# Performance work log

Hardware: AMD Instinct MI355X
Metric: run time of the kernel (lower is better)

Reference implementation:

```python
import jax, jax.numpy as jnp
import numpy as np

B, T, I, H, O = 128, 1024, 128, 1024, 128

def setup_inputs() -> dict:
    key = jax.random.key(0)
    ks = jax.random.split(key, 11)
    s = 1.0 / np.sqrt(H)  # torch default LSTM init scale
    return {
        "x": jax.random.normal(ks[0], (B, T, I), jnp.float32),
        "sequence_length": jax.random.randint(ks[1], (B,), 0, T, jnp.int64 if jax.config.jax_enable_x64 else jnp.int32),
        "hn": jax.random.normal(ks[2], (B, H), jnp.float32),
        "cn": jax.random.normal(ks[3], (B, H), jnp.float32),
        "output_t": jax.random.normal(ks[4], (B, O), jnp.float32),
        "W_ih": jax.random.normal(ks[5], (4 * H, I + O), jnp.float32) * s,
        "W_hh": jax.random.normal(ks[6], (4 * H, H), jnp.float32) * s,
        "b_ih": jax.random.normal(ks[7], (4 * H,), jnp.float32) * s,
        "b_hh": jax.random.normal(ks[8], (4 * H,), jnp.float32) * s,
        "W_out": jax.random.normal(ks[9], (O, H), jnp.float32) * s,
        "b_out": jax.random.normal(ks[10], (O,), jnp.float32) * s,
    }

def reference(x, sequence_length, hn, cn, output_t, W_ih, W_hh, b_ih, b_hh, W_out, b_out):
    # eval mode (self.training=False): no dropout applied
    Tn = x.shape[1]
    Hd = hn.shape[-1]
    # masks[t, b] = 1.0 if sequence_length[b] > t
    masks = (jnp.arange(Tn)[:, None] < sequence_length[None, :]).astype(x.dtype)  # [T, B]
    xs = jnp.transpose(x, (1, 0, 2))  # [T, B, I]
    bias = b_ih + b_hh

    def step(carry, inp):
        h, c, out_t = carry
        xt, m = inp                      # xt [B,I], m [B]
        m = m[:, None]                   # [B,1]
        lstm_in = jnp.concatenate([xt * m, out_t], axis=-1)  # [B, I+O]
        gates = lstm_in @ W_ih.T + h @ W_hh.T + bias          # [B, 4H]
        i_g, f_g, g_g, o_g = jnp.split(gates, 4, axis=-1)     # torch gate order i,f,g,o
        i_g = jax.nn.sigmoid(i_g)
        f_g = jax.nn.sigmoid(f_g)
        g_g = jnp.tanh(g_g)
        o_g = jax.nn.sigmoid(o_g)
        c = f_g * c + i_g * g_g
        h = o_g * jnp.tanh(c)
        out_t = h @ W_out.T + b_out      # [B, O]
        return (h, c, out_t), out_t * m

    (_, _, _), ys = jax.lax.scan(step, (hn, cn, output_t), (xs, masks))
    return jnp.transpose(ys, (1, 0, 2))  # [B, T, O]
```

## Files before the change

kernel.cpp:

```cpp
#include <hip/hip_runtime.h>
#include <stdint.h>

#define Tn 1024
#define In 128

typedef __attribute__((ext_vector_type(8))) short short8;
typedef __attribute__((ext_vector_type(4))) float f32x4;
typedef unsigned long long u64;

#define WS_WFRAG  0ull
#define WS_WOUT   (WS_WFRAG + 10485760ull)
#define WS_Z0     (WS_WOUT + 262144ull)
#define WS_HBUF   (WS_Z0 + 32768ull)
#define WS_BIAS   (WS_HBUF + 524288ull)
#define WS_CNT    (WS_BIAS + 16384ull)

__device__ __forceinline__ unsigned short f2bf(float f) {
  unsigned u = __builtin_bit_cast(unsigned, f);
  return (unsigned short)((u + 0x7FFFu + ((u >> 16) & 1u)) >> 16);
}
__device__ __forceinline__ float fast_sig(float v) {
  float e = __builtin_amdgcn_exp2f(-1.44269504089f * v);
  return __builtin_amdgcn_rcpf(1.0f + e);
}
__device__ __forceinline__ float fast_tanh(float v) {
  float a = fabsf(v);
  float e = __builtin_amdgcn_exp2f(-2.88539008178f * a);
  float r = (1.0f - e) * __builtin_amdgcn_rcpf(1.0f + e);
  return copysignf(r, v);
}

__global__ void k_wfrag(const float* __restrict__ Wih, const float* __restrict__ Whh,
                        const float* __restrict__ Wout, char* __restrict__ ws) {
  const int u = blockIdx.x, nt = blockIdx.y, kt = blockIdx.z;
  const int lane = threadIdx.x;
  const int col = lane & 15, quad = lane >> 4;
  const int n = (col & 3) * 1024 + u * 32 + nt * 4 + (col >> 2);
  float v[8];
  if (kt < 32) {
    const int k = kt * 32 + quad * 8;
    #pragma unroll
    for (int e = 0; e < 8; e++) v[e] = Whh[(size_t)n * 1024 + k + e];
    const float* wo = Wih + (size_t)n * 256 + 128;
    for (int o = 0; o < 128; o++) {
      const float wv = wo[o];
      const float* wr = Wout + (size_t)o * 1024 + k;
      #pragma unroll
      for (int e = 0; e < 8; e++) v[e] = fmaf(wv, wr[e], v[e]);
    }
  } else if (kt < 36) {
    const int k = (kt - 32) * 32 + quad * 8;
    #pragma unroll
    for (int e = 0; e < 8; e++) v[e] = Wih[(size_t)n * 256 + k + e];
  } else {
    const int o = (kt - 36) * 32 + quad * 8;
    #pragma unroll
    for (int e = 0; e < 8; e++) v[e] = Wih[(size_t)n * 256 + 128 + o + e];
  }
  short8 pk;
  #pragma unroll
  for (int e = 0; e < 8; e++) pk[e] = (short)f2bf(v[e]);
  *(short8*)(ws + WS_WFRAG + ((size_t)((u * 8 + nt) * 40 + kt) * 64 + lane) * 16) = pk;
}

__global__ void k_misc(const float* __restrict__ Wout, const float* __restrict__ hn,
                       const float* __restrict__ out_t, const float* __restrict__ bout,
                       const float* __restrict__ bih, const float* __restrict__ bhh,
                       const float* __restrict__ Wih, float* __restrict__ outp,
                       char* __restrict__ ws) {
  const int blk = blockIdx.x, lane = threadIdx.x;
  const int col = lane & 15, quad = lane >> 4;
  if (blk < 256) {
    const int u = blk >> 5, kt = blk & 31;
    const int o = u * 16 + col, j0 = kt * 32 + quad * 8;
    short8 pk;
    #pragma unroll
    for (int e = 0; e < 8; e++) pk[e] = (short)f2bf(Wout[(size_t)o * 1024 + j0 + e]);
    *(short8*)(ws + WS_WOUT + ((size_t)(u * 32 + kt) * 64 + lane) * 16) = pk;
  } else if (blk < 512) {
    const int t2 = blk - 256;
    const int mm = t2 >> 5, kt = t2 & 31;
    const int b = mm * 16 + col, j0 = kt * 32 + quad * 8;
    short8 pk;
    #pragma unroll
    for (int e = 0; e < 8; e++) pk[e] = (short)f2bf(hn[(size_t)b * 1024 + j0 + e]);
    *(short8*)(ws + WS_HBUF + ((size_t)((8 + mm) * 32 + kt) * 64 + lane) * 16) = pk;
  } else if (blk < 544) {
    const int t2 = blk - 512;
    const int mm = t2 >> 2, kz = t2 & 3;
    const int b = mm * 16 + col;
    const int o0 = kz * 32 + quad * 8;
    float acc[8];
    #pragma unroll
    for (int e = 0; e < 8; e++) acc[e] = out_t[(size_t)b * 128 + o0 + e] - bout[o0 + e];
    for (int j = 0; j < 1024; j += 4) {
      const f32x4 h4 = *(const f32x4*)(hn + (size_t)b * 1024 + j);
      #pragma unroll
      for (int e = 0; e < 8; e++) {
        const f32x4 w4 = *(const f32x4*)(Wout + (size_t)(o0 + e) * 1024 + j);
        acc[e] -= h4[0] * w4[0] + h4[1] * w4[1] + h4[2] * w4[2] + h4[3] * w4[3];
      }
    }
    short8 pk;
    #pragma unroll
    for (int e = 0; e < 8; e++) pk[e] = (short)f2bf(acc[e]);
    *(short8*)(ws + WS_Z0 + ((size_t)(mm * 4 + kz) * 64 + lane) * 16) = pk;
  } else if (blk < 608) {
    const int n = (blk - 544) * 64 + lane;
    float v = bih[n] + bhh[n];
    const float* wo = Wih + (size_t)n * 256 + 128;
    for (int o = 0; o < 128; o++) v = fmaf(wo[o], bout[o], v);
    ((float*)(ws + WS_BIAS))[n] = v;
  } else if (blk < 616) {
    int* c = (int*)(ws + WS_CNT);
    const int base = ((blk - 608) * 64 + lane) * 16;
    #pragma unroll
    for (int k = 0; k < 16; k++) c[base + k] = 0;
  } else {
    int* c = (int*)outp;
    #pragma unroll
    for (int k = 0; k < 8; k++) c[lane * 8 + k] = 0;
  }
}

__launch_bounds__(512, 2)
__global__ void k_main(const float* __restrict__ x, const int* __restrict__ seq,
                       const float* __restrict__ cn, const float* __restrict__ b_out,
                       float* __restrict__ out, char* __restrict__ ws) {
  __shared__ short8 a_lds[40 * 64];
  __shared__ short8 htile[64];
  __shared__ float  ysred[8 * 16 * 20];
  __shared__ float  bo_lds[16];
  __shared__ int    seq_lds[16];

  const int tid  = threadIdx.x;
  const int lane = tid & 63;
  const int w    = tid >> 6;
  const int wg   = blockIdx.x;

  int* cnt = (int*)(ws + WS_CNT);

  int m_, u_, fast_;
  {
    int* ids = (int*)ysred;
    int* scr = (int*)out;
    if (tid == 0) {
      int myxcd;
      asm volatile("s_getreg_b32 %0, hwreg(HW_REG_XCC_ID)" : "=s"(myxcd));
      myxcd &= 7;
      ids[259] = myxcd;
      __hip_atomic_store(&scr[8 + wg], myxcd, __ATOMIC_RELAXED, __HIP_MEMORY_SCOPE_SYSTEM);
      __hip_atomic_fetch_add(&scr[0], 1, __ATOMIC_ACQ_REL, __HIP_MEMORY_SCOPE_SYSTEM);
      while (__hip_atomic_load(&scr[0], __ATOMIC_ACQUIRE, __HIP_MEMORY_SCOPE_SYSTEM) < 256) {}
    }
    __syncthreads();
    if (tid < 256)
      ids[tid] = __hip_atomic_load(&scr[8 + tid], __ATOMIC_RELAXED,
                                   __HIP_MEMORY_SCOPE_SYSTEM) & 7;
    __syncthreads();
    if (tid == 0) {
      const int myxcd = ids[259];
      int cx[8] = {0, 0, 0, 0, 0, 0, 0, 0};
      int rank = 0;
      for (int i = 0; i < 256; i++) {
        const int xi = ids[i];
        cx[xi]++;
        if (xi == myxcd && i < wg) rank++;
      }
      bool bal = true;
      for (int k = 0; k < 8; k++) bal = bal && (cx[k] == 32);
      ids[256] = bal ? myxcd : (wg & 7);
      ids[257] = bal ? rank : (wg >> 3);
      ids[258] = bal ? 1 : 0;
      __hip_atomic_fetch_add(&scr[1], 1, __ATOMIC_ACQ_REL, __HIP_MEMORY_SCOPE_SYSTEM);
      while (__hip_atomic_load(&scr[1], __ATOMIC_ACQUIRE, __HIP_MEMORY_SCOPE_SYSTEM) < 256) {}
    }
    __syncthreads();
    m_ = ids[256]; u_ = ids[257]; fast_ = ids[258];
    __syncthreads();
  }
  const int  m     = m_;
  const int  u     = u_;
  const bool fastp = (fast_ != 0);

  const char* wfrag = ws + WS_WFRAG;
  const char* woutf = ws + WS_WOUT;
  char* hbuf  = ws + WS_HBUF;
  const float* bias2 = (const float*)(ws + WS_BIAS);

  short8 bfr[40];
  {
    const char* base = wfrag + ((size_t)(u * 8 + w) * 40 * 64) * 16 + (size_t)lane * 16;
    #pragma unroll
    for (int kt = 0; kt < 40; kt++) bfr[kt] = *(const short8*)(base + (size_t)kt * 1024);
  }
  if (tid < 16) seq_lds[tid] = seq[m * 16 + tid];
  if (tid < 16 && u < 8) bo_lds[tid] = b_out[u * 16 + tid];

  const int col16 = lane & 15;
  const int quad  = lane >> 4;
  const int jj_my = w * 4 + quad;
  float bias_g[4];
  #pragma unroll
  for (int j = 0; j < 4; j++) bias_g[j] = bias2[j * 1024 + u * 32 + jj_my];
  float c_reg = cn[(size_t)(m * 16 + col16) * 1024 + u * 32 + jj_my];
  __syncthreads();

  #pragma unroll 1
  for (int tt = 0; tt <= Tn; tt++) {
    if (tt < Tn && tid < 256) {
      const int kt4 = tid >> 6, ln = tid & 63;
      const int b = ln & 15, qd = ln >> 4;
      const int i0 = kt4 * 32 + qd * 8;
      const float* xp = x + ((size_t)(m * 16 + b) * Tn + tt) * In + i0;
      const float mk = (tt < seq_lds[b]) ? 1.0f : 0.0f;
      const f32x4 x0 = *(const f32x4*)xp;
      const f32x4 x1 = *(const f32x4*)(xp + 4);
      short8 pk;
      pk[0] = (short)f2bf(x0[0] * mk); pk[1] = (short)f2bf(x0[1] * mk);
      pk[2] = (short)f2bf(x0[2] * mk); pk[3] = (short)f2bf(x0[3] * mk);
      pk[4] = (short)f2bf(x1[0] * mk); pk[5] = (short)f2bf(x1[1] * mk);
      pk[6] = (short)f2bf(x1[2] * mk); pk[7] = (short)f2bf(x1[3] * mk);
      a_lds[(32 + kt4) * 64 + ln] = pk;
    }
    if (tt == 0 && tid < 256) {
      const int kz = tid >> 6, ln = tid & 63;
      a_lds[(36 + kz) * 64 + ln] =
          *(const short8*)(ws + WS_Z0 + ((size_t)(m * 4 + kz) * 64 + ln) * 16);
    }
    if (tt >= 1 && tid == 0) {
      while (__hip_atomic_load(&cnt[m * 1024 + (tt - 1)], __ATOMIC_RELAXED,
                               __HIP_MEMORY_SCOPE_SYSTEM) < 32) {}
    }
    __syncthreads();
    {
      const char* srcb = hbuf + (size_t)((((tt + 1) & 1) * 8) + m) * 32768;
      if (fastp && tt >= 1) {
        const f32x4* sp = (const f32x4*)srcb;
        f32x4 t0, t1, t2, t3;
        asm volatile(
            "global_load_dwordx4 %0, %4, off sc0\n\t"
            "global_load_dwordx4 %1, %5, off sc0\n\t"
            "global_load_dwordx4 %2, %6, off sc0\n\t"
            "global_load_dwordx4 %3, %7, off sc0\n\t"
            "s_waitcnt vmcnt(0)"
            : "=&v"(t0), "=&v"(t1), "=&v"(t2), "=&v"(t3)
            : "v"(sp + tid), "v"(sp + 512 + tid), "v"(sp + 1024 + tid),
              "v"(sp + 1536 + tid)
            : "memory");
        f32x4* dst = (f32x4*)a_lds;
        dst[tid] = t0; dst[512 + tid] = t1; dst[1024 + tid] = t2; dst[1536 + tid] = t3;
      } else {
        const u64* src = (const u64*)srcb;
        u64 tmp[8];
        #pragma unroll
        for (int s = 0; s < 8; s++)
          tmp[s] = __hip_atomic_load(&src[s * 512 + tid], __ATOMIC_RELAXED,
                                     __HIP_MEMORY_SCOPE_SYSTEM);
        u64* dst = (u64*)a_lds;
        #pragma unroll
        for (int s = 0; s < 8; s++) dst[s * 512 + tid] = tmp[s];
      }
    }
    __syncthreads();

    if (tt < Tn) {
      f32x4 acc0 = {bias_g[0], bias_g[1], bias_g[2], bias_g[3]};
      f32x4 acc1 = {0.f, 0.f, 0.f, 0.f};
      f32x4 acc2 = {0.f, 0.f, 0.f, 0.f};
      f32x4 acc3 = {0.f, 0.f, 0.f, 0.f};
      #pragma unroll
      for (int kk = 0; kk < 9; kk++) {
        const short8 a0 = a_lds[(kk * 4 + 0) * 64 + lane];
        const short8 a1 = a_lds[(kk * 4 + 1) * 64 + lane];
        const short8 a2 = a_lds[(kk * 4 + 2) * 64 + lane];
        const short8 a3 = a_lds[(kk * 4 + 3) * 64 + lane];
        acc0 = __builtin_amdgcn_mfma_f32_16x16x32_bf16(bfr[kk * 4 + 0], a0, acc0, 0, 0, 0);
        acc1 = __builtin_amdgcn_mfma_f32_16x16x32_bf16(bfr[kk * 4 + 1], a1, acc1, 0, 0, 0);
        acc2 = __builtin_amdgcn_mfma_f32_16x16x32_bf16(bfr[kk * 4 + 2], a2, acc2, 0, 0, 0);
        acc3 = __builtin_amdgcn_mfma_f32_16x16x32_bf16(bfr[kk * 4 + 3], a3, acc3, 0, 0, 0);
      }
      if (tt == 0) {
        const short8 z0 = a_lds[36 * 64 + lane];
        const short8 z1 = a_lds[37 * 64 + lane];
        const short8 z2 = a_lds[38 * 64 + lane];
        const short8 z3 = a_lds[39 * 64 + lane];
        acc0 = __builtin_amdgcn_mfma_f32_16x16x32_bf16(bfr[36], z0, acc0, 0, 0, 0);
        acc1 = __builtin_amdgcn_mfma_f32_16x16x32_bf16(bfr[37], z1, acc1, 0, 0, 0);
        acc2 = __builtin_amdgcn_mfma_f32_16x16x32_bf16(bfr[38], z2, acc2, 0, 0, 0);
        acc3 = __builtin_amdgcn_mfma_f32_16x16x32_bf16(bfr[39], z3, acc3, 0, 0, 0);
      }
      {
        const float Gi = acc0[0] + acc1[0] + acc2[0] + acc3[0];
        const float Gf = acc0[1] + acc1[1] + acc2[1] + acc3[1];
        const float Gg = acc0[2] + acc1[2] + acc2[2] + acc3[2];
        const float Go = acc0[3] + acc1[3] + acc2[3] + acc3[3];
        const float ig = fast_sig(Gi), fg = fast_sig(Gf);
        const float gg = fast_tanh(Gg), og = fast_sig(Go);
        c_reg = fg * c_reg + ig * gg;
        const float h = og * fast_tanh(c_reg);
        ((short*)htile)[(col16 + 16 * (jj_my >> 3)) * 8 + (jj_my & 7)] = (short)f2bf(h);
      }
      __syncthreads();
      if (tid < 64) {
        const short8 v = htile[lane];
        char* dstb = hbuf + (size_t)((tt & 1) * 8 + m) * 32768 + (size_t)u * 1024 +
                     (size_t)lane * 16;
        if (fastp) {
          asm volatile("global_store_dwordx4 %0, %1, off sc0" :: "v"(dstb), "v"(v)
                       : "memory");
        } else {
          u64* dstp = (u64*)dstb;
          const u64* pv = (const u64*)&v;
          __hip_atomic_store(&dstp[0], pv[0], __ATOMIC_RELAXED, __HIP_MEMORY_SCOPE_SYSTEM);
          __hip_atomic_store(&dstp[1], pv[1], __ATOMIC_RELAXED, __HIP_MEMORY_SCOPE_SYSTEM);
        }
        asm volatile("s_waitcnt vmcnt(0)" ::: "memory");
        if (tid == 0)
          __hip_atomic_fetch_add(&cnt[m * 1024 + tt], 1, __ATOMIC_RELAXED,
                                 __HIP_MEMORY_SCOPE_SYSTEM);
      }
    }

    if (u < 8 && tt >= 1) {
      f32x4 yacc = {0.f, 0.f, 0.f, 0.f};
      const char* wob = woutf + ((size_t)(u * 32 + w * 4) * 64 + lane) * 16;
      #pragma unroll
      for (int i = 0; i < 4; i++) {
        const short8 bf = *(const short8*)(wob + (size_t)i * 1024);
        const short8 af = a_lds[(w * 4 + i) * 64 + lane];
        yacc = __builtin_amdgcn_mfma_f32_16x16x32_bf16(af, bf, yacc, 0, 0, 0);
      }
      {
        const int o = lane & 15, bq = (lane >> 4) * 4;
        *(f32x4*)&ysred[(w * 16 + o) * 20 + bq] = yacc;
      }
      __syncthreads();
      if (tid < 256) {
        const int o = tid & 15, b = tid >> 4;
        float s = 0.f;
        #pragma unroll
        for (int q = 0; q < 8; q++) s += ysred[(q * 16 + o) * 20 + b];
        s += bo_lds[o];
        const float val = ((tt - 1) < seq_lds[b]) ? s : 0.0f;
        out[((size_t)(m * 16 + b) * Tn + (tt - 1)) * 128 + u * 16 + o] = val;
      }
      __syncthreads();
    }
  }
}

extern "C" void kernel_launch(void* const* d_in, const int* in_sizes, int n_in,
                              void* d_out, int out_size, void* d_ws, size_t ws_size,
                              hipStream_t stream) {
  (void)in_sizes; (void)n_in; (void)out_size; (void)ws_size;
  const float* x    = (const float*)d_in[0];
  const int*   seq  = (const int*)d_in[1];
  const float* hn   = (const float*)d_in[2];
  const float* cn   = (const float*)d_in[3];
  const float* outt = (const float*)d_in[4];
  const float* Wih  = (const float*)d_in[5];
  const float* Whh  = (const float*)d_in[6];
  const float* bih  = (const float*)d_in[7];
  const float* bhh  = (const float*)d_in[8];
  const float* Wout = (const float*)d_in[9];
  const float* bout = (const float*)d_in[10];
  float* out = (float*)d_out;
  char* ws = (char*)d_ws;

  hipLaunchKernelGGL(k_wfrag, dim3(32, 8, 40), dim3(64), 0, stream, Wih, Whh, Wout, ws);
  hipLaunchKernelGGL(k_misc, dim3(617), dim3(64), 0, stream, Wout, hn, outt, bout,
                     bih, bhh, Wih, out, ws);
  void* args[] = {(void*)&x, (void*)&seq, (void*)&cn, (void*)&bout, (void*)&out, (void*)&ws};
  hipLaunchCooperativeKernel((const void*)k_main, dim3(256), dim3(512), args, 0, stream);
}
```

Measured before the change: 3.088 ms.

## Interleave two batch groups per workgroup to overlap compute with cross-block sync

Each workgroup now handles two 16-row batch groups (p*2, p*2+1). Half the waves run the gate MFMAs for one group while the other half run the output projection for the other group, so one group's barrier wait overlaps the other's compute. Each group spans 64 workgroups instead of 32 and waits for 64 arrivals. The XCC-id discovery and placement handshake is removed, along with the sc0 fast load/store path; all h exchange now uses system-scope atomic u64 accesses. This trades cross-XCD locality and the cheaper load path for latency hiding, with more barriers per step and wider synchronisation fan-in.

```diff
diff --git a/kernel.cpp b/kernel.cpp
--- a/kernel.cpp
+++ b/kernel.cpp
@@ -111,16 +111,13 @@
     const float* wo = Wih + (size_t)n * 256 + 128;
     for (int o = 0; o < 128; o++) v = fmaf(wo[o], bout[o], v);
     ((float*)(ws + WS_BIAS))[n] = v;
-  } else if (blk < 616) {
+  } else {
     int* c = (int*)(ws + WS_CNT);
     const int base = ((blk - 608) * 64 + lane) * 16;
     #pragma unroll
     for (int k = 0; k < 16; k++) c[base + k] = 0;
-  } else {
-    int* c = (int*)outp;
-    #pragma unroll
-    for (int k = 0; k < 8; k++) c[lane * 8 + k] = 0;
   }
+  (void)outp;
 }
 
 __launch_bounds__(512, 2)
@@ -128,82 +125,42 @@
                        const float* __restrict__ cn, const float* __restrict__ b_out,
                        float* __restrict__ out, char* __restrict__ ws) {
   __shared__ short8 a_lds[40 * 64];
-  __shared__ short8 htile[64];
-  __shared__ float  ysred[8 * 16 * 20];
+  __shared__ u64    htile[64];
+  __shared__ float  ysred[4 * 16 * 20];
   __shared__ float  bo_lds[16];
-  __shared__ int    seq_lds[16];
+  __shared__ int    seq_lds[32];
 
   const int tid  = threadIdx.x;
   const int lane = tid & 63;
   const int w    = tid >> 6;
   const int wg   = blockIdx.x;
+  const int p    = wg >> 6;
+  const int v    = wg & 63;
+  const int grp  = w >> 2;
+  const int wt   = w & 3;
+  const int col16 = lane & 15, quad = lane >> 4;
+  const int ut   = v * 4 + wt;
+  const int junit = ut * 4 + quad;
+  const int gA = p * 2, gB = p * 2 + 1;
 
   int* cnt = (int*)(ws + WS_CNT);
-
-  int m_, u_, fast_;
-  {
-    int* ids = (int*)ysred;
-    int* scr = (int*)out;
-    if (tid == 0) {
-      int myxcd;
-      asm volatile("s_getreg_b32 %0, hwreg(HW_REG_XCC_ID)" : "=s"(myxcd));
-      myxcd &= 7;
-      ids[259] = myxcd;
-      __hip_atomic_store(&scr[8 + wg], myxcd, __ATOMIC_RELAXED, __HIP_MEMORY_SCOPE_SYSTEM);
-      __hip_atomic_fetch_add(&scr[0], 1, __ATOMIC_ACQ_REL, __HIP_MEMORY_SCOPE_SYSTEM);
-      while (__hip_atomic_load(&scr[0], __ATOMIC_ACQUIRE, __HIP_MEMORY_SCOPE_SYSTEM) < 256) {}
-    }
-    __syncthreads();
-    if (tid < 256)
-      ids[tid] = __hip_atomic_load(&scr[8 + tid], __ATOMIC_RELAXED,
-                                   __HIP_MEMORY_SCOPE_SYSTEM) & 7;
-    __syncthreads();
-    if (tid == 0) {
-      const int myxcd = ids[259];
-      int cx[8] = {0, 0, 0, 0, 0, 0, 0, 0};
-      int rank = 0;
-      for (int i = 0; i < 256; i++) {
-        const int xi = ids[i];
-        cx[xi]++;
-        if (xi == myxcd && i < wg) rank++;
-      }
-      bool bal = true;
-      for (int k = 0; k < 8; k++) bal = bal && (cx[k] == 32);
-      ids[256] = bal ? myxcd : (wg & 7);
-      ids[257] = bal ? rank : (wg >> 3);
-      ids[258] = bal ? 1 : 0;
-      __hip_atomic_fetch_add(&scr[1], 1, __ATOMIC_ACQ_REL, __HIP_MEMORY_SCOPE_SYSTEM);
-      while (__hip_atomic_load(&scr[1], __ATOMIC_ACQUIRE, __HIP_MEMORY_SCOPE_SYSTEM) < 256) {}
-    }
-    __syncthreads();
-    m_ = ids[256]; u_ = ids[257]; fast_ = ids[258];
-    __syncthreads();
-  }
-  const int  m     = m_;
-  const int  u     = u_;
-  const bool fastp = (fast_ != 0);
-
   const char* wfrag = ws + WS_WFRAG;
   const char* woutf = ws + WS_WOUT;
-  char* hbuf  = ws + WS_HBUF;
+  char* hbuf = ws + WS_HBUF;
   const float* bias2 = (const float*)(ws + WS_BIAS);
 
   short8 bfr[40];
   {
-    const char* base = wfrag + ((size_t)(u * 8 + w) * 40 * 64) * 16 + (size_t)lane * 16;
+    const char* base = wfrag + ((size_t)ut * 40 * 64) * 16 + (size_t)lane * 16;
     #pragma unroll
     for (int kt = 0; kt < 40; kt++) bfr[kt] = *(const short8*)(base + (size_t)kt * 1024);
   }
-  if (tid < 16) seq_lds[tid] = seq[m * 16 + tid];
-  if (tid < 16 && u < 8) bo_lds[tid] = b_out[u * 16 + tid];
-
-  const int col16 = lane & 15;
-  const int quad  = lane >> 4;
-  const int jj_my = w * 4 + quad;
+  if (tid < 32) seq_lds[tid] = seq[p * 32 + tid];
+  if (tid < 16 && v < 16) bo_lds[tid] = b_out[(v & 7) * 16 + tid];
   float bias_g[4];
   #pragma unroll
-  for (int j = 0; j < 4; j++) bias_g[j] = bias2[j * 1024 + u * 32 + jj_my];
-  float c_reg = cn[(size_t)(m * 16 + col16) * 1024 + u * 32 + jj_my];
+  for (int j = 0; j < 4; j++) bias_g[j] = bias2[j * 1024 + junit];
+  float c_reg = cn[(size_t)(p * 32 + grp * 16 + col16) * 1024 + junit];
   __syncthreads();
 
   #pragma unroll 1
@@ -212,7 +169,7 @@
       const int kt4 = tid >> 6, ln = tid & 63;
       const int b = ln & 15, qd = ln >> 4;
       const int i0 = kt4 * 32 + qd * 8;
-      const float* xp = x + ((size_t)(m * 16 + b) * Tn + tt) * In + i0;
+      const float* xp = x + ((size_t)(p * 32 + b) * Tn + tt) * In + i0;
       const float mk = (tt < seq_lds[b]) ? 1.0f : 0.0f;
       const f32x4 x0 = *(const f32x4*)xp;
       const f32x4 x1 = *(const f32x4*)(xp + 4);
@@ -223,48 +180,29 @@
       pk[6] = (short)f2bf(x1[2] * mk); pk[7] = (short)f2bf(x1[3] * mk);
       a_lds[(32 + kt4) * 64 + ln] = pk;
     }
-    if (tt == 0 && tid < 256) {
-      const int kz = tid >> 6, ln = tid & 63;
+    if (tt == 0 && tid >= 256) {
+      const int kz = (tid - 256) >> 6, ln = tid & 63;
       a_lds[(36 + kz) * 64 + ln] =
-          *(const short8*)(ws + WS_Z0 + ((size_t)(m * 4 + kz) * 64 + ln) * 16);
+          *(const short8*)(ws + WS_Z0 + ((size_t)(gA * 4 + kz) * 64 + ln) * 16);
     }
     if (tt >= 1 && tid == 0) {
-      while (__hip_atomic_load(&cnt[m * 1024 + (tt - 1)], __ATOMIC_RELAXED,
-                               __HIP_MEMORY_SCOPE_SYSTEM) < 32) {}
+      while (__hip_atomic_load(&cnt[gA * 1024 + (tt - 1)], __ATOMIC_RELAXED,
+                               __HIP_MEMORY_SCOPE_SYSTEM) < 64) {}
     }
     __syncthreads();
     {
-      const char* srcb = hbuf + (size_t)((((tt + 1) & 1) * 8) + m) * 32768;
-      if (fastp && tt >= 1) {
-        const f32x4* sp = (const f32x4*)srcb;
-        f32x4 t0, t1, t2, t3;
-        asm volatile(
-            "global_load_dwordx4 %0, %4, off sc0\n\t"
-            "global_load_dwordx4 %1, %5, off sc0\n\t"
-            "global_load_dwordx4 %2, %6, off sc0\n\t"
-            "global_load_dwordx4 %3, %7, off sc0\n\t"
-            "s_waitcnt vmcnt(0)"
-            : "=&v"(t0), "=&v"(t1), "=&v"(t2), "=&v"(t3)
-            : "v"(sp + tid), "v"(sp + 512 + tid), "v"(sp + 1024 + tid),
-              "v"(sp + 1536 + tid)
-            : "memory");
-        f32x4* dst = (f32x4*)a_lds;
-        dst[tid] = t0; dst[512 + tid] = t1; dst[1024 + tid] = t2; dst[1536 + tid] = t3;
-      } else {
-        const u64* src = (const u64*)srcb;
-        u64 tmp[8];
-        #pragma unroll
-        for (int s = 0; s < 8; s++)
-          tmp[s] = __hip_atomic_load(&src[s * 512 + tid], __ATOMIC_RELAXED,
-                                     __HIP_MEMORY_SCOPE_SYSTEM);
-        u64* dst = (u64*)a_lds;
-        #pragma unroll
-        for (int s = 0; s < 8; s++) dst[s * 512 + tid] = tmp[s];
-      }
-    }
-    __syncthreads();
-
-    if (tt < Tn) {
+      const u64* src = (const u64*)(hbuf + (size_t)((((tt + 1) & 1) * 8) + gA) * 32768);
+      u64 tmp[8];
+      #pragma unroll
+      for (int s = 0; s < 8; s++)
+        tmp[s] = __hip_atomic_load(&src[s * 512 + tid], __ATOMIC_RELAXED,
+                                   __HIP_MEMORY_SCOPE_SYSTEM);
+      u64* dst = (u64*)a_lds;
+      #pragma unroll
+      for (int s = 0; s < 8; s++) dst[s * 512 + tid] = tmp[s];
+    }
+    __syncthreads();
+    if (tt < Tn && grp == 0) {
       f32x4 acc0 = {bias_g[0], bias_g[1], bias_g[2], bias_g[3]};
       f32x4 acc1 = {0.f, 0.f, 0.f, 0.f};
       f32x4 acc2 = {0.f, 0.f, 0.f, 0.f};
@@ -290,63 +228,156 @@
         acc2 = __builtin_amdgcn_mfma_f32_16x16x32_bf16(bfr[38], z2, acc2, 0, 0, 0);
         acc3 = __builtin_amdgcn_mfma_f32_16x16x32_bf16(bfr[39], z3, acc3, 0, 0, 0);
       }
-      {
-        const float Gi = acc0[0] + acc1[0] + acc2[0] + acc3[0];
-        const float Gf = acc0[1] + acc1[1] + acc2[1] + acc3[1];
-        const float Gg = acc0[2] + acc1[2] + acc2[2] + acc3[2];
-        const float Go = acc0[3] + acc1[3] + acc2[3] + acc3[3];
-        const float ig = fast_sig(Gi), fg = fast_sig(Gf);
-        const float gg = fast_tanh(Gg), og = fast_sig(Go);
-        c_reg = fg * c_reg + ig * gg;
-        const float h = og * fast_tanh(c_reg);
-        ((short*)htile)[(col16 + 16 * (jj_my >> 3)) * 8 + (jj_my & 7)] = (short)f2bf(h);
-      }
-      __syncthreads();
-      if (tid < 64) {
-        const short8 v = htile[lane];
-        char* dstb = hbuf + (size_t)((tt & 1) * 8 + m) * 32768 + (size_t)u * 1024 +
-                     (size_t)lane * 16;
-        if (fastp) {
-          asm volatile("global_store_dwordx4 %0, %1, off sc0" :: "v"(dstb), "v"(v)
-                       : "memory");
-        } else {
-          u64* dstp = (u64*)dstb;
-          const u64* pv = (const u64*)&v;
-          __hip_atomic_store(&dstp[0], pv[0], __ATOMIC_RELAXED, __HIP_MEMORY_SCOPE_SYSTEM);
-          __hip_atomic_store(&dstp[1], pv[1], __ATOMIC_RELAXED, __HIP_MEMORY_SCOPE_SYSTEM);
-        }
-        asm volatile("s_waitcnt vmcnt(0)" ::: "memory");
-        if (tid == 0)
-          __hip_atomic_fetch_add(&cnt[m * 1024 + tt], 1, __ATOMIC_RELAXED,
-                                 __HIP_MEMORY_SCOPE_SYSTEM);
-      }
-    }
-
-    if (u < 8 && tt >= 1) {
+      const float Gi = acc0[0] + acc1[0] + acc2[0] + acc3[0];
+      const float Gf = acc0[1] + acc1[1] + acc2[1] + acc3[1];
+      const float Gg = acc0[2] + acc1[2] + acc2[2] + acc3[2];
+      const float Go = acc0[3] + acc1[3] + acc2[3] + acc3[3];
+      const float ig = fast_sig(Gi), fg = fast_sig(Gf);
+      const float gg = fast_tanh(Gg), og = fast_sig(Go);
+      c_reg = fg * c_reg + ig * gg;
+      const float h = og * fast_tanh(c_reg);
+      const int jl = wt * 4 + quad;
+      ((short*)htile)[((jl >> 3) * 16 + col16) * 8 + (jl & 7)] = (short)f2bf(h);
+    }
+    if (tt >= 1 && grp == 1 && v < 8) {
       f32x4 yacc = {0.f, 0.f, 0.f, 0.f};
-      const char* wob = woutf + ((size_t)(u * 32 + w * 4) * 64 + lane) * 16;
-      #pragma unroll
-      for (int i = 0; i < 4; i++) {
-        const short8 bf = *(const short8*)(wob + (size_t)i * 1024);
-        const short8 af = a_lds[(w * 4 + i) * 64 + lane];
+      #pragma unroll
+      for (int i = 0; i < 8; i++) {
+        const int kt = wt * 8 + i;
+        const short8 bf = *(const short8*)(woutf + ((size_t)(v * 32 + kt) * 64 + lane) * 16);
+        const short8 af = a_lds[kt * 64 + lane];
         yacc = __builtin_amdgcn_mfma_f32_16x16x32_bf16(af, bf, yacc, 0, 0, 0);
       }
-      {
-        const int o = lane & 15, bq = (lane >> 4) * 4;
-        *(f32x4*)&ysred[(w * 16 + o) * 20 + bq] = yacc;
-      }
-      __syncthreads();
-      if (tid < 256) {
-        const int o = tid & 15, b = tid >> 4;
-        float s = 0.f;
-        #pragma unroll
-        for (int q = 0; q < 8; q++) s += ysred[(q * 16 + o) * 20 + b];
-        s += bo_lds[o];
-        const float val = ((tt - 1) < seq_lds[b]) ? s : 0.0f;
-        out[((size_t)(m * 16 + b) * Tn + (tt - 1)) * 128 + u * 16 + o] = val;
-      }
-      __syncthreads();
-    }
+      *(f32x4*)&ysred[(wt * 16 + (lane & 15)) * 20 + (lane >> 4) * 4] = yacc;
+    }
+    __syncthreads();
+    if (tt < Tn && w == 0) {
+      const u64 hv = htile[lane];
+      u64* dstp = (u64*)(hbuf + (size_t)((tt & 1) * 8 + gA) * 32768 +
+                         (size_t)v * 512 + (size_t)lane * 8);
+      __hip_atomic_store(dstp, hv, __ATOMIC_RELAXED, __HIP_MEMORY_SCOPE_SYSTEM);
+      asm volatile("s_waitcnt vmcnt(0)" ::: "memory");
+      if (tid == 0)
+        __hip_atomic_fetch_add(&cnt[gA * 1024 + tt], 1, __ATOMIC_RELAXED,
+                               __HIP_MEMORY_SCOPE_SYSTEM);
+    }
+    if (tt >= 1 && v < 8 && tid >= 256) {
+      const int idx = tid - 256;
+      const int o = idx & 15, b = idx >> 4;
+      float s = 0.f;
+      #pragma unroll
+      for (int q = 0; q < 4; q++) s += ysred[(q * 16 + o) * 20 + b];
+      s += bo_lds[o];
+      const float val = ((tt - 1) < seq_lds[b]) ? s : 0.0f;
+      out[((size_t)(p * 32 + b) * Tn + (tt - 1)) * 128 + v * 16 + o] = val;
+    }
+    if (tt == 0 && tid >= 256) {
+      const int kz = (tid - 256) >> 6, ln = tid & 63;
+      a_lds[(36 + kz) * 64 + ln] =
+          *(const short8*)(ws + WS_Z0 + ((size_t)(gB * 4 + kz) * 64 + ln) * 16);
+    }
+    if (tt >= 1 && tid == 64) {
+      while (__hip_atomic_load(&cnt[gB * 1024 + (tt - 1)], __ATOMIC_RELAXED,
+                               __HIP_MEMORY_SCOPE_SYSTEM) < 64) {}
+    }
+    __syncthreads();
+    {
+      const u64* src = (const u64*)(hbuf + (size_t)((((tt + 1) & 1) * 8) + gB) * 32768);
+      u64 tmp[8];
+      #pragma unroll
+      for (int s = 0; s < 8; s++)
+        tmp[s] = __hip_atomic_load(&src[s * 512 + tid], __ATOMIC_RELAXED,
+                                   __HIP_MEMORY_SCOPE_SYSTEM);
+      u64* dst = (u64*)a_lds;
+      #pragma unroll
+      for (int s = 0; s < 8; s++) dst[s * 512 + tid] = tmp[s];
+    }
+    if (tt < Tn && tid < 256) {
+      const int kt4 = tid >> 6, ln = tid & 63;
+      const int b = ln & 15, qd = ln >> 4;
+      const int i0 = kt4 * 32 + qd * 8;
+      const float* xp = x + ((size_t)(p * 32 + 16 + b) * Tn + tt) * In + i0;
+      const float mk = (tt < seq_lds[16 + b]) ? 1.0f : 0.0f;
+      const f32x4 x0 = *(const f32x4*)xp;
+      const f32x4 x1 = *(const f32x4*)(xp + 4);
+      short8 pk;
+      pk[0] = (short)f2bf(x0[0] * mk); pk[1] = (short)f2bf(x0[1] * mk);
+      pk[2] = (short)f2bf(x0[2] * mk); pk[3] = (short)f2bf(x0[3] * mk);
+      pk[4] = (short)f2bf(x1[0] * mk); pk[5] = (short)f2bf(x1[1] * mk);
+      pk[6] = (short)f2bf(x1[2] * mk); pk[7] = (short)f2bf(x1[3] * mk);
+      a_lds[(32 + kt4) * 64 + ln] = pk;
+    }
+    __syncthreads();
+    if (tt < Tn && grp == 1) {
+      f32x4 acc0 = {bias_g[0], bias_g[1], bias_g[2], bias_g[3]};
+      f32x4 acc1 = {0.f, 0.f, 0.f, 0.f};
+      f32x4 acc2 = {0.f, 0.f, 0.f, 0.f};
+      f32x4 acc3 = {0.f, 0.f, 0.f, 0.f};
+      #pragma unroll
+      for (int kk = 0; kk < 9; kk++) {
+        const short8 a0 = a_lds[(kk * 4 + 0) * 64 + lane];
+        const short8 a1 = a_lds[(kk * 4 + 1) * 64 + lane];
+        const short8 a2 = a_lds[(kk * 4 + 2) * 64 + lane];
+        const short8 a3 = a_lds[(kk * 4 + 3) * 64 + lane];
+        acc0 = __builtin_amdgcn_mfma_f32_16x16x32_bf16(bfr[kk * 4 + 0], a0, acc0, 0, 0, 0);
+        acc1 = __builtin_amdgcn_mfma_f32_16x16x32_bf16(bfr[kk * 4 + 1], a1, acc1, 0, 0, 0);
+        acc2 = __builtin_amdgcn_mfma_f32_16x16x32_bf16(bfr[kk * 4 + 2], a2, acc2, 0, 0, 0);
+        acc3 = __builtin_amdgcn_mfma_f32_16x16x32_bf16(bfr[kk * 4 + 3], a3, acc3, 0, 0, 0);
+      }
+      if (tt == 0) {
+        const short8 z0 = a_lds[36 * 64 + lane];
+        const short8 z1 = a_lds[37 * 64 + lane];
+        const short8 z2 = a_lds[38 * 64 + lane];
+        const short8 z3 = a_lds[39 * 64 + lane];
+        acc0 = __builtin_amdgcn_mfma_f32_16x16x32_bf16(bfr[36], z0, acc0, 0, 0, 0);
+        acc1 = __builtin_amdgcn_mfma_f32_16x16x32_bf16(bfr[37], z1, acc1, 0, 0, 0);
+        acc2 = __builtin_amdgcn_mfma_f32_16x16x32_bf16(bfr[38], z2, acc2, 0, 0, 0);
+        acc3 = __builtin_amdgcn_mfma_f32_16x16x32_bf16(bfr[39], z3, acc3, 0, 0, 0);
+      }
+      const float Gi = acc0[0] + acc1[0] + acc2[0] + acc3[0];
+      const float Gf = acc0[1] + acc1[1] + acc2[1] + acc3[1];
+      const float Gg = acc0[2] + acc1[2] + acc2[2] + acc3[2];
+      const float Go = acc0[3] + acc1[3] + acc2[3] + acc3[3];
+      const float ig = fast_sig(Gi), fg = fast_sig(Gf);
+      const float gg = fast_tanh(Gg), og = fast_sig(Go);
+      c_reg = fg * c_reg + ig * gg;
+      const float h = og * fast_tanh(c_reg);
+      const int jl = wt * 4 + quad;
+      ((short*)htile)[((jl >> 3) * 16 + col16) * 8 + (jl & 7)] = (short)f2bf(h);
+    }
+    if (tt >= 1 && grp == 0 && v >= 8 && v < 16) {
+      f32x4 yacc = {0.f, 0.f, 0.f, 0.f};
+      #pragma unroll
+      for (int i = 0; i < 8; i++) {
+        const int kt = wt * 8 + i;
+        const short8 bf =
+            *(const short8*)(woutf + ((size_t)((v - 8) * 32 + kt) * 64 + lane) * 16);
+        const short8 af = a_lds[kt * 64 + lane];
+        yacc = __builtin_amdgcn_mfma_f32_16x16x32_bf16(af, bf, yacc, 0, 0, 0);
+      }
+      *(f32x4*)&ysred[(wt * 16 + (lane & 15)) * 20 + (lane >> 4) * 4] = yacc;
+    }
+    __syncthreads();
+    if (tt < Tn && w == 4) {
+      const u64 hv = htile[lane];
+      u64* dstp = (u64*)(hbuf + (size_t)((tt & 1) * 8 + gB) * 32768 +
+                         (size_t)v * 512 + (size_t)lane * 8);
+      __hip_atomic_store(dstp, hv, __ATOMIC_RELAXED, __HIP_MEMORY_SCOPE_SYSTEM);
+      asm volatile("s_waitcnt vmcnt(0)" ::: "memory");
+      if (tid == 256)
+        __hip_atomic_fetch_add(&cnt[gB * 1024 + tt], 1, __ATOMIC_RELAXED,
+                               __HIP_MEMORY_SCOPE_SYSTEM);
+    }
+    if (tt >= 1 && v >= 8 && v < 16 && tid < 256) {
+      const int o = tid & 15, b = tid >> 4;
+      float s = 0.f;
+      #pragma unroll
+      for (int q = 0; q < 4; q++) s += ysred[(q * 16 + o) * 20 + b];
+      s += bo_lds[o];
+      const float val = ((tt - 1) < seq_lds[16 + b]) ? s : 0.0f;
+      out[((size_t)(p * 32 + 16 + b) * Tn + (tt - 1)) * 128 + (v - 8) * 16 + o] = val;
+    }
+    __syncthreads();
   }
 }
 
@@ -369,7 +400,7 @@
   char* ws = (char*)d_ws;
 
   hipLaunchKernelGGL(k_wfrag, dim3(32, 8, 40), dim3(64), 0, stream, Wih, Whh, Wout, ws);
-  hipLaunchKernelGGL(k_misc, dim3(617), dim3(64), 0, stream, Wout, hn, outt, bout,
+  hipLaunchKernelGGL(k_misc, dim3(616), dim3(64), 0, stream, Wout, hn, outt, bout,
                      bih, bhh, Wih, out, ws);
   void* args[] = {(void*)&x, (void*)&seq, (void*)&cn, (void*)&bout, (void*)&out, (void*)&ws};
   hipLaunchCooperativeKernel((const void*)k_main, dim3(256), dim3(512), args, 0, stream);
```

Measured after the change: 6.511 ms. +110.9%, slower.
